# Kernel tuning notes

Hardware: AMD Instinct MI355X
Metric: run time of the kernel (lower is better)

The kernel has to match this reference:

```python
import jax, jax.numpy as jnp
import numpy as np

EPSILON = 1e-8
K = 3
PAD = K // 2


def setup_inputs() -> dict:
    key = jax.random.key(0)
    k1, k2, k3, k4 = jax.random.split(key, 4)
    B, FI, FO, H, W, DSTYLE = 8, 512, 512, 64, 64, 512
    return {
        "x": jax.random.normal(k1, (B, FI, H, W), dtype=jnp.float32),
        "style": jax.random.normal(k2, (B, DSTYLE), dtype=jnp.float32),
        "w": jax.random.normal(k3, (FO, FI, K, K), dtype=jnp.float32),
        "fc_w": jax.random.normal(k4, (FI, DSTYLE), dtype=jnp.float32),  # modLinear weight [dim_out=fi, dim_in=dim_style]
        "fc_b": jnp.zeros((FI,), dtype=jnp.float32),
    }


def reference(x, style, w, fc_w, fc_b):
    B, FI, H, W = x.shape
    FO = w.shape[0]
    DSTYLE = fc_w.shape[1]
    fc_scale = DSTYLE ** (-0.5)            # modLinear w_scale (lr_mult=1)
    w_scale = (FI * K * K) ** (-0.5)       # modConv w_scale

    # modLinear: style -> per-input-channel modulation s, shape [B, FI]
    s = style @ (fc_w * fc_scale).T + fc_b

    # Demod factor: d[b, fo] = rsqrt(sum_{fi,k,k} (w_scale * w * s[b,fi])^2 + eps)
    wsq = jnp.sum((w * w_scale) ** 2, axis=(2, 3))          # [FO, FI]
    d = jax.lax.rsqrt(jnp.einsum('of,bf->bo', wsq, s ** 2) + EPSILON)  # [B, FO]

    # Equivalent to per-sample grouped conv: scale input channels by s,
    # conv with shared base weight, scale output channels by demod.
    xm = x * s[:, :, None, None]
    y = jax.lax.conv_general_dilated(
        xm, w * w_scale,
        window_strides=(1, 1),
        padding=((PAD, PAD), (PAD, PAD)),
        dimension_numbers=('NCHW', 'OIHW', 'NCHW'),
    )
    return y * d[:, :, None, None]
```

## Files before the change

### kernel.cpp

```cpp
#include <hip/hip_runtime.h>


typedef __bf16 bf16_t;
typedef __bf16 bf16x8 __attribute__((ext_vector_type(8)));
typedef float floatx4 __attribute__((ext_vector_type(4)));

#define HW_ 4096
#define FCSCALE 0.04419417382415922f
#define WSCALE  0.014731391274719742f

#define VMCNT(n) asm volatile("s_waitcnt vmcnt(" #n ")" ::: "memory")

__device__ __forceinline__ void gload_lds16(const bf16_t* g, bf16_t* l) {
  __builtin_amdgcn_global_load_lds(
      (const __attribute__((address_space(1))) void*)g,
      (__attribute__((address_space(3))) void*)l, 16, 0, 0);
}


__device__ __forceinline__ void style_body(int bid, int t,
    const float* __restrict__ style, const float* __restrict__ fc_w,
    const float* __restrict__ fc_b, float* __restrict__ s_out) {
  int o = bid * 4 + (t >> 6);
  int lane = t & 63;
  int b = o >> 9, fi = o & 511;
  const float4* st = (const float4*)(style + b * 512);
  const float4* fw = (const float4*)(fc_w + (size_t)fi * 512);
  float4 a0 = st[lane * 2],     w0 = fw[lane * 2];
  float4 a1 = st[lane * 2 + 1], w1 = fw[lane * 2 + 1];
  float acc = a0.x * w0.x + a0.y * w0.y + a0.z * w0.z + a0.w * w0.w
            + a1.x * w1.x + a1.y * w1.y + a1.z * w1.z + a1.w * w1.w;
#pragma unroll
  for (int d = 32; d >= 1; d >>= 1) acc += __shfl_xor(acc, d, 64);
  if (lane == 0) s_out[o] = acc * FCSCALE + fc_b[fi];
}

__device__ __forceinline__ void wsq_wt_body(int bid, int t,
    const float* __restrict__ w, float* __restrict__ wsq, bf16_t* __restrict__ wt) {
  int idx = bid * 256 + t;
  int fo = idx >> 9, fi = idx & 511;
  const float* wp = w + (size_t)idx * 9;
  float v[9], q = 0.f;
#pragma unroll
  for (int k = 0; k < 9; ++k) { v[k] = wp[k] * WSCALE; q += v[k] * v[k]; }
  wsq[idx] = q;
#pragma unroll
  for (int k = 0; k < 9; ++k)
    wt[((((size_t)k * 64) + (fi >> 3)) * 512 + fo) * 8 + (fi & 7)] = (bf16_t)v[k];
}

__device__ __forceinline__ void demod_body(int bid, int t,
    const float* __restrict__ wsq, const float* __restrict__ s,
    float* __restrict__ dcoef) {
  int o = bid * 4 + (t >> 6);
  int lane = t & 63;
  int b = o >> 9, fo = o & 511;
  const float4* wq = (const float4*)(wsq + (size_t)fo * 512);
  const float4* sp = (const float4*)(s + b * 512);
  float acc = 0.f;
#pragma unroll
  for (int i = 0; i < 2; ++i) {
    float4 q = wq[lane * 2 + i], sv = sp[lane * 2 + i];
    acc += q.x * sv.x * sv.x + q.y * sv.y * sv.y + q.z * sv.z * sv.z + q.w * sv.w * sv.w;
  }
#pragma unroll
  for (int d = 32; d >= 1; d >>= 1) acc += __shfl_xor(acc, d, 64);
  if (lane == 0) dcoef[o] = rsqrtf(acc + 1e-8f);
}

__global__ void k_prep1(const float* __restrict__ style, const float* __restrict__ fc_w,
                        const float* __restrict__ fc_b, const float* __restrict__ w,
                        float* __restrict__ s_out, float* __restrict__ wsq,
                        bf16_t* __restrict__ wt, bf16_t* __restrict__ zerobuf) {
  int blk = blockIdx.x, t = threadIdx.x;
  if (blk < 1024) {
    wsq_wt_body(blk, t, w, wsq, wt);
  } else if (blk < 2048) {
    style_body(blk - 1024, t, style, fc_w, fc_b, s_out);
  } else {
    if (t < 128) zerobuf[t] = (bf16_t)0.f;
  }
}

__device__ __forceinline__ void modx_body(int fi0, int h, int b, int t,
    const float* __restrict__ x, const float* __restrict__ s,
    bf16_t* __restrict__ xT, float (*tile)[65]) {
  int c4 = (t & 15) * 4, fr = t >> 4;
#pragma unroll
  for (int i = 0; i < 2; ++i) {
    int fi_l = i * 16 + fr;
    float sv = s[b * 512 + fi0 + fi_l];
    float4 v = *(const float4*)(x + ((size_t)(b * 512 + fi0 + fi_l)) * HW_ + h * 64 + c4);
    tile[fi_l][c4] = v.x * sv; tile[fi_l][c4 + 1] = v.y * sv;
    tile[fi_l][c4 + 2] = v.z * sv; tile[fi_l][c4 + 3] = v.w * sv;
  }
  __syncthreads();
  int g_l = t >> 6, wcol = t & 63;
  bf16x8 vv;
#pragma unroll
  for (int j = 0; j < 8; ++j) vv[j] = (bf16_t)tile[g_l * 8 + j][wcol];
  *(bf16x8*)&xT[((((size_t)(b * 64 + h)) * 64 + (fi0 >> 3) + g_l) * 64 + wcol) * 8] = vv;
}

__global__ void k_prep2(const float* __restrict__ x, const float* __restrict__ s,
                        const float* __restrict__ wsq, float* __restrict__ dcoef,
                        bf16_t* __restrict__ xT) {
  __shared__ float tile[32][65];
  int blk = blockIdx.x, t = threadIdx.x;
  if (blk < 1024) {
    demod_body(blk, t, wsq, s, dcoef);
  } else {
    int m = blk - 1024;
    int b = m >> 10, rem = m & 1023;
    int h = rem >> 4, fi0 = (rem & 15) * 32;
    modx_body(fi0, h, b, t, x, s, xT, tile);
  }
}

__global__ __launch_bounds__(256, 2) void k_conv(const bf16_t* __restrict__ wt,
                                                 const bf16_t* __restrict__ xT,
                                                 const float* __restrict__ dcoef,
                                                 const bf16_t* __restrict__ zerobuf,
                                                 float* __restrict__ out) {
  __shared__ __align__(16) bf16_t sh[32776];

  int b   = blockIdx.x;
  int foB = blockIdx.y;
  int hq  = blockIdx.z;
  int t = threadIdx.x;
  int wv = t >> 6, lane = t & 63, quad = lane >> 4, l16 = lane & 15;
  int h0 = hq * 4;
  int fo_l = t & 127, chunk_hi = t >> 7;

  const bf16_t* xTb = xT + (size_t)b * 64 * 64 * 64 * 8;
  const bf16_t* zslotp = &sh[32768];
  int XRB = ((wv * 4 + quad) * 64 + l16) * 8;

  floatx4 acc[8][4];
#pragma unroll
  for (int i = 0; i < 8; ++i)
#pragma unroll
    for (int j = 0; j < 4; ++j) acc[i][j] = (floatx4){0.f, 0.f, 0.f, 0.f};

  if (t < 8) sh[32768 + t] = (bf16_t)0.f;
#pragma unroll
  for (int k = 0; k < 3; ++k)
#pragma unroll
    for (int u = 0; u < 2; ++u) {
      int s = k * 8 + wv * 2 + u;
      int r = s >> 2, g = s & 3;
      int rg = h0 + r - 1;
      const bf16_t* src = ((unsigned)rg < 64u)
          ? xTb + (((size_t)rg * 64 + g) * 64 + lane) * 8
          : zerobuf;
      gload_lds16(src, &sh[((r * 4 + g) * 64) * 8]);
    }
#pragma unroll
  for (int itw = 0; itw < 2; ++itw) {
    int cw = itw * 2 + chunk_hi;
    gload_lds16(wt + (((size_t)cw) * 512 + foB * 128 + fo_l) * 8,
                &sh[24576 + (itw * 256 + wv * 64) * 8]);
  }
  VMCNT(0);
  __syncthreads();

#define PHASE(P, NW, XPART, GCLAST)                                            \
  do {                                                                         \
    VMCNT(NW);                                                                 \
    __builtin_amdgcn_s_barrier();                                              \
    __builtin_amdgcn_sched_barrier(0);                                         \
    if (!(GCLAST) || (P) < 8) {        \
      const int TAP1 = ((P) + 1) % 9;                                          \
      int g01 = ((P) == 8) ? (gc + 1) * 4 : gc * 4;                            \
      int wb1 = ((gc9 + (P) + 1) & 1) * 4096;                                  \
      _Pragma("unroll")                                                        \
      for (int itw = 0; itw < 2; ++itw) {                                      \
        int cw = itw * 2 + chunk_hi;                                           \
        gload_lds16(wt + ((((size_t)TAP1 * 64) + g01 + cw) * 512               \
                          + foB * 128 + fo_l) * 8,                             \
                    &sh[24576 + wb1 + (itw * 256 + wv * 64) * 8]);             \
      }                                                                        \
    }                                                                          \
    if ((XPART) >= 0 && !(GCLAST)) { \
      int xb1 = ((gc + 1) & 1) * 12288;                                        \
      int g0n = (gc + 1) * 4;                                                  \
      _Pragma("unroll")                                                        \
      for (int u = 0; u < 2; ++u) {                                            \
        int s = (XPART) * 8 + wv * 2 + u;                                      \
        int r = s >> 2, g = s & 3;                                             \
        int rg = h0 + r - 1;                                                   \
        const bf16_t* src = ((unsigned)rg < 64u)                               \
            ? xTb + (((size_t)rg * 64 + g0n + g) * 64 + lane) * 8              \
            : zerobuf;                                                         \
        gload_lds16(src, &sh[xb1 + ((r * 4 + g) * 64) * 8]);                   \
      }                                                                        \
    }                                                                          \
    {                                  \
      const int KH = (P) / 3, KW = (P) % 3;                                    \
      int xb = (gc & 1) * 12288;                                               \
      int wb = ((gc9 + (P)) & 1) * 4096;                                       \
      bf16x8 bfr[4];                                                           \
      _Pragma("unroll")                                                        \
      for (int j = 0; j < 4; ++j) {                                            \
        const bf16_t* ap = &sh[xb + XRB + KH * 2048 + (j * 16 + KW - 1) * 8];  \
        if (KW == 0 && (j) == 0) { if (l16 == 0)  ap = zslotp; }               \
        if (KW == 2 && (j) == 3) { if (l16 == 15) ap = zslotp; }               \
        bfr[j] = *(const bf16x8*)ap;                                           \
      }                                                                        \
      __builtin_amdgcn_s_setprio(1);                                           \
      _Pragma("unroll")                                                        \
      for (int i = 0; i < 8; ++i) {                                            \
        bf16x8 afr = *(const bf16x8*)&sh[24576 + wb                            \
                                         + (quad * 128 + i * 16 + l16) * 8];   \
        _Pragma("unroll")                                                      \
        for (int j = 0; j < 4; ++j)                                            \
          acc[i][j] = __builtin_amdgcn_mfma_f32_16x16x32_bf16(                 \
              afr, bfr[j], acc[i][j], 0, 0, 0);                                \
      }                                                                        \
      __builtin_amdgcn_s_setprio(0);                                           \
    }                                                                          \
  } while (0)

  for (int gc = 0; gc < 15; ++gc) {
    int gc9 = gc * 9;
    PHASE(0, 0, -1, false);
    PHASE(1, 0,  0, false);
    PHASE(2, 2,  1, false);
    PHASE(3, 2,  2, false);
    PHASE(4, 2, -1, false);
    PHASE(5, 0, -1, false);
    PHASE(6, 0, -1, false);
    PHASE(7, 0, -1, false);
    PHASE(8, 0, -1, false);
  }
  {
    int gc = 15, gc9 = 135;
    PHASE(0, 0, -1, true);
    PHASE(1, 0, -1, true);
    PHASE(2, 0, -1, true);
    PHASE(3, 0, -1, true);
    PHASE(4, 0, -1, true);
    PHASE(5, 0, -1, true);
    PHASE(6, 0, -1, true);
    PHASE(7, 0, -1, true);
    PHASE(8, 0, -1, true);
  }
#undef PHASE

  int h = h0 + wv;
#pragma unroll
  for (int i = 0; i < 8; ++i) {
#pragma unroll
    for (int rr = 0; rr < 4; ++rr) {
      int fo_g = foB * 128 + i * 16 + quad * 4 + rr;
      float dm = dcoef[b * 512 + fo_g];
      float* op = out + ((size_t)((b * 512 + fo_g) * 64 + h)) * 64;
#pragma unroll
      for (int j = 0; j < 4; ++j)
        op[j * 16 + l16] = acc[i][j][rr] * dm;
    }
  }
}

extern "C" void kernel_launch(void* const* d_in, const int* in_sizes, int n_in,
                              void* d_out, int out_size, void* d_ws, size_t ws_size,
                              hipStream_t stream) {
  const float* x     = (const float*)d_in[0];
  const float* style = (const float*)d_in[1];
  const float* w     = (const float*)d_in[2];
  const float* fc_w  = (const float*)d_in[3];
  const float* fc_b  = (const float*)d_in[4];
  float* out = (float*)d_out;
  char* ws = (char*)d_ws;

  float*  s       = (float*)(ws);
  float*  dcoef   = (float*)(ws + 16384);
  float*  wsq     = (float*)(ws + 32768);
  bf16_t* zerobuf = (bf16_t*)(ws + 1081344);
  bf16_t* wt      = (bf16_t*)(ws + 1081600);
  bf16_t* xT      = (bf16_t*)(ws + 5800192);

  k_prep1<<<2049, 256, 0, stream>>>(style, fc_w, fc_b, w, s, wsq, wt, zerobuf);
  k_prep2<<<9216, 256, 0, stream>>>(x, s, wsq, dcoef, xT);
  k_conv<<<dim3(8, 4, 16), 256, 0, stream>>>(wt, xT, dcoef, zerobuf, out);
}
```

Baseline: 235.4 us.

## Stream conv weights into registers and retile waves to cut barriers

Weight fragments no longer go through LDS. Each wave loads them straight from global memory into a double-buffered register array, one tap ahead of the MFMA work. The waves are retiled as 2 output-channel halves by 2 row pairs, each wave holding 4x8 accumulators, and the workgroup barrier now runs only twice per pair of input-channel chunks instead of once per tap. This is meant to remove the per-tap barrier and LDS weight staging and to shrink LDS use. The cost is redundant global/L2 weight traffic across waves and exposed global-load latency in the register pipeline.

```diff
diff --git a/kernel.cpp b/kernel.cpp
--- a/kernel.cpp
+++ b/kernel.cpp
@@ -122,7 +122,7 @@
                                                  const float* __restrict__ dcoef,
                                                  const bf16_t* __restrict__ zerobuf,
                                                  float* __restrict__ out) {
-  __shared__ __align__(16) bf16_t sh[32776];
+  __shared__ __align__(16) bf16_t sh[24584];
 
   int b   = blockIdx.x;
   int foB = blockIdx.y;
@@ -130,25 +130,29 @@
   int t = threadIdx.x;
   int wv = t >> 6, lane = t & 63, quad = lane >> 4, l16 = lane & 15;
   int h0 = hq * 4;
-  int fo_l = t & 127, chunk_hi = t >> 7;
+  int rowpair = (wv >> 1) * 2;
+  int foW = foB * 128 + (wv & 1) * 64;
 
   const bf16_t* xTb = xT + (size_t)b * 64 * 64 * 64 * 8;
-  const bf16_t* zslotp = &sh[32768];
-  int XRB = ((wv * 4 + quad) * 64 + l16) * 8;
-
-  floatx4 acc[8][4];
-#pragma unroll
-  for (int i = 0; i < 8; ++i)
-#pragma unroll
-    for (int j = 0; j < 4; ++j) acc[i][j] = (floatx4){0.f, 0.f, 0.f, 0.f};
-
-  if (t < 8) sh[32768 + t] = (bf16_t)0.f;
-#pragma unroll
-  for (int k = 0; k < 3; ++k)
+  const bf16_t* wA_base = wt + ((size_t)(quad * 512 + foW + l16)) * 8;
+  const bf16_t* xlbase = &sh[(quad * 64 + l16) * 8];
+  const bf16_t* zslotp = &sh[24576];
+
+  floatx4 acc[4][8];
+#pragma unroll
+  for (int i = 0; i < 4; ++i)
+#pragma unroll
+    for (int j = 0; j < 8; ++j) acc[i][j] = (floatx4){0.f, 0.f, 0.f, 0.f};
+
+  bf16x8 aF[2][4];
+
+  if (t < 8) sh[24576 + t] = (bf16_t)0.f;
+#pragma unroll
+  for (int part = 0; part < 3; ++part)
 #pragma unroll
     for (int u = 0; u < 2; ++u) {
-      int s = k * 8 + wv * 2 + u;
-      int r = s >> 2, g = s & 3;
+      int sp = part * 8 + wv * 2 + u;
+      int r = sp >> 2, g = sp & 3;
       int rg = h0 + r - 1;
       const bf16_t* src = ((unsigned)rg < 64u)
           ? xTb + (((size_t)rg * 64 + g) * 64 + lane) * 8
@@ -156,108 +160,92 @@
       gload_lds16(src, &sh[((r * 4 + g) * 64) * 8]);
     }
 #pragma unroll
-  for (int itw = 0; itw < 2; ++itw) {
-    int cw = itw * 2 + chunk_hi;
-    gload_lds16(wt + (((size_t)cw) * 512 + foB * 128 + fo_l) * 8,
-                &sh[24576 + (itw * 256 + wv * 64) * 8]);
-  }
+  for (int i = 0; i < 4; ++i)
+    aF[0][i] = *(const bf16x8*)(wA_base + i * 128);
   VMCNT(0);
   __syncthreads();
 
-#define PHASE(P, NW, XPART, GCLAST)                                            \
+#define PH(IT18, LAST)                                                         \
   do {                                                                         \
-    VMCNT(NW);                                                                 \
-    __builtin_amdgcn_s_barrier();                                              \
-    __builtin_amdgcn_sched_barrier(0);                                         \
-    if (!(GCLAST) || (P) < 8) {        \
-      const int TAP1 = ((P) + 1) % 9;                                          \
-      int g01 = ((P) == 8) ? (gc + 1) * 4 : gc * 4;                            \
-      int wb1 = ((gc9 + (P) + 1) & 1) * 4096;                                  \
-      _Pragma("unroll")                                                        \
-      for (int itw = 0; itw < 2; ++itw) {                                      \
-        int cw = itw * 2 + chunk_hi;                                           \
-        gload_lds16(wt + ((((size_t)TAP1 * 64) + g01 + cw) * 512               \
-                          + foB * 128 + fo_l) * 8,                             \
-                    &sh[24576 + wb1 + (itw * 256 + wv * 64) * 8]);             \
-      }                                                                        \
-    }                                                                          \
-    if ((XPART) >= 0 && !(GCLAST)) { \
-      int xb1 = ((gc + 1) & 1) * 12288;                                        \
-      int g0n = (gc + 1) * 4;                                                  \
+    const int TAP_ = (IT18) % 9;                                               \
+    const int GH_  = (IT18) / 9;                                               \
+    if ((IT18) == 0 || (IT18) == 9) {                                          \
+      VMCNT(4);                                       \
+      __builtin_amdgcn_s_barrier();                 \
+      __builtin_amdgcn_sched_barrier(0);                                       \
+    }                                                                          \
+    if (TAP_ >= 3 && TAP_ <= 5 && !((LAST) && GH_ == 1)) {                     \
+      int gcn = gbase + GH_ + 1;                \
+      int xb1 = (gcn & 1) * 12288;                                             \
       _Pragma("unroll")                                                        \
       for (int u = 0; u < 2; ++u) {                                            \
-        int s = (XPART) * 8 + wv * 2 + u;                                      \
-        int r = s >> 2, g = s & 3;                                             \
+        int sp = (TAP_ - 3) * 8 + wv * 2 + u;                                  \
+        int r = sp >> 2, g = sp & 3;                                           \
         int rg = h0 + r - 1;                                                   \
         const bf16_t* src = ((unsigned)rg < 64u)                               \
-            ? xTb + (((size_t)rg * 64 + g0n + g) * 64 + lane) * 8              \
+            ? xTb + (((size_t)rg * 64 + gcn * 4 + g) * 64 + lane) * 8          \
             : zerobuf;                                                         \
         gload_lds16(src, &sh[xb1 + ((r * 4 + g) * 64) * 8]);                   \
       }                                                                        \
     }                                                                          \
-    {                                  \
-      const int KH = (P) / 3, KW = (P) % 3;                                    \
-      int xb = (gc & 1) * 12288;                                               \
-      int wb = ((gc9 + (P)) & 1) * 4096;                                       \
-      bf16x8 bfr[4];                                                           \
+    if (!((LAST) && (IT18) == 17)) {             \
+      const int T1 = ((IT18) + 1) % 9;                                         \
+      const int C1 = ((IT18) + 1) / 9;                                         \
+      const bf16_t* pA = wA_base + (size_t)(T1 * 64 + (gbase + C1) * 4) * 4096;\
       _Pragma("unroll")                                                        \
-      for (int j = 0; j < 4; ++j) {                                            \
-        const bf16_t* ap = &sh[xb + XRB + KH * 2048 + (j * 16 + KW - 1) * 8];  \
-        if (KW == 0 && (j) == 0) { if (l16 == 0)  ap = zslotp; }               \
-        if (KW == 2 && (j) == 3) { if (l16 == 15) ap = zslotp; }               \
-        bfr[j] = *(const bf16x8*)ap;                                           \
-      }                                                                        \
+      for (int i = 0; i < 4; ++i)                                              \
+        aF[((IT18) + 1) & 1][i] = *(const bf16x8*)(pA + i * 128);              \
+    }                                                                          \
+    {                                         \
+      const int KH_ = TAP_ / 3, KW_ = TAP_ % 3;                                \
+      const int XO_ = GH_ * 12288;                                             \
       __builtin_amdgcn_s_setprio(1);                                           \
       _Pragma("unroll")                                                        \
-      for (int i = 0; i < 8; ++i) {                                            \
-        bf16x8 afr = *(const bf16x8*)&sh[24576 + wb                            \
-                                         + (quad * 128 + i * 16 + l16) * 8];   \
+      for (int j = 0; j < 8; ++j) {                                            \
+        int r = rowpair + (j >> 2) + KH_;                                      \
+        const bf16_t* ap =                                                     \
+            xlbase + XO_ + r * 2048 + ((j & 3) * 16 + KW_ - 1) * 8;            \
+        if (KW_ == 0 && (j & 3) == 0) { if (l16 == 0)  ap = zslotp; }          \
+        if (KW_ == 2 && (j & 3) == 3) { if (l16 == 15) ap = zslotp; }          \
+        bf16x8 bfr = *(const bf16x8*)ap;                                       \
         _Pragma("unroll")                                                      \
-        for (int j = 0; j < 4; ++j)                                            \
+        for (int i = 0; i < 4; ++i)                                            \
           acc[i][j] = __builtin_amdgcn_mfma_f32_16x16x32_bf16(                 \
-              afr, bfr[j], acc[i][j], 0, 0, 0);                                \
+              aF[(IT18) & 1][i], bfr, acc[i][j], 0, 0, 0);                     \
       }                                                                        \
       __builtin_amdgcn_s_setprio(0);                                           \
     }                                                                          \
   } while (0)
 
-  for (int gc = 0; gc < 15; ++gc) {
-    int gc9 = gc * 9;
-    PHASE(0, 0, -1, false);
-    PHASE(1, 0,  0, false);
-    PHASE(2, 2,  1, false);
-    PHASE(3, 2,  2, false);
-    PHASE(4, 2, -1, false);
-    PHASE(5, 0, -1, false);
-    PHASE(6, 0, -1, false);
-    PHASE(7, 0, -1, false);
-    PHASE(8, 0, -1, false);
+  for (int gcp = 0; gcp < 7; ++gcp) {
+    int gbase = gcp * 2;
+    PH(0, false);  PH(1, false);  PH(2, false);  PH(3, false);  PH(4, false);
+    PH(5, false);  PH(6, false);  PH(7, false);  PH(8, false);  PH(9, false);
+    PH(10, false); PH(11, false); PH(12, false); PH(13, false); PH(14, false);
+    PH(15, false); PH(16, false); PH(17, false);
   }
   {
-    int gc = 15, gc9 = 135;
-    PHASE(0, 0, -1, true);
-    PHASE(1, 0, -1, true);
-    PHASE(2, 0, -1, true);
-    PHASE(3, 0, -1, true);
-    PHASE(4, 0, -1, true);
-    PHASE(5, 0, -1, true);
-    PHASE(6, 0, -1, true);
-    PHASE(7, 0, -1, true);
-    PHASE(8, 0, -1, true);
-  }
-#undef PHASE
-
-  int h = h0 + wv;
-#pragma unroll
-  for (int i = 0; i < 8; ++i) {
+    int gbase = 14;
+    PH(0, true);  PH(1, true);  PH(2, true);  PH(3, true);  PH(4, true);
+    PH(5, true);  PH(6, true);  PH(7, true);  PH(8, true);  PH(9, true);
+    PH(10, true); PH(11, true); PH(12, true); PH(13, true); PH(14, true);
+    PH(15, true); PH(16, true); PH(17, true);
+  }
+#undef PH
+
+#pragma unroll
+  for (int i = 0; i < 4; ++i) {
 #pragma unroll
     for (int rr = 0; rr < 4; ++rr) {
-      int fo_g = foB * 128 + i * 16 + quad * 4 + rr;
+      int fo_g = foW + i * 16 + quad * 4 + rr;
       float dm = dcoef[b * 512 + fo_g];
-      float* op = out + ((size_t)((b * 512 + fo_g) * 64 + h)) * 64;
-#pragma unroll
-      for (int j = 0; j < 4; ++j)
-        op[j * 16 + l16] = acc[i][j][rr] * dm;
+      float* op = out + ((size_t)(b * 512 + fo_g)) * 4096;
+#pragma unroll
+      for (int j = 0; j < 8; ++j) {
+        int h = h0 + rowpair + (j >> 2);
+        int c = (j & 3) * 16 + l16;
+        op[h * 64 + c] = acc[i][j][rr] * dm;
+      }
     }
   }
 }
```

Result: slower. 282.5 us (+20.0%).

## Double weight prefetch to two taps per barrier and unroll channel-group pairs

Applied to the files above, without the earlier changes.

Restructures the conv main loop so weight tiles for two taps are loaded together into a larger double-buffered LDS region, and a barrier is issued only every other MFMA phase. Two channel groups are processed per loop iteration, with x-tile prefetches rescheduled to match. The zero-slot pointer trick for boundary columns is replaced with wrapped LDS reads plus a register select of a zero vector. The aim is to halve barrier and wait overhead and deepen prefetch, at the cost of more LDS (80KB per block), which may lower occupancy from 2 blocks per CU.

```diff
diff --git a/kernel.cpp b/kernel.cpp
--- a/kernel.cpp
+++ b/kernel.cpp
@@ -122,7 +122,7 @@
                                                  const float* __restrict__ dcoef,
                                                  const bf16_t* __restrict__ zerobuf,
                                                  float* __restrict__ out) {
-  __shared__ __align__(16) bf16_t sh[32776];
+  __shared__ __align__(16) bf16_t sh[40960];
 
   int b   = blockIdx.x;
   int foB = blockIdx.y;
@@ -133,7 +133,6 @@
   int fo_l = t & 127, chunk_hi = t >> 7;
 
   const bf16_t* xTb = xT + (size_t)b * 64 * 64 * 64 * 8;
-  const bf16_t* zslotp = &sh[32768];
   int XRB = ((wv * 4 + quad) * 64 + l16) * 8;
 
   floatx4 acc[8][4];
@@ -142,13 +141,16 @@
 #pragma unroll
     for (int j = 0; j < 4; ++j) acc[i][j] = (floatx4){0.f, 0.f, 0.f, 0.f};
 
-  if (t < 8) sh[32768 + t] = (bf16_t)0.f;
-#pragma unroll
-  for (int k = 0; k < 3; ++k)
+  bf16x8 z8;
+#pragma unroll
+  for (int q = 0; q < 8; ++q) z8[q] = (bf16_t)0.f;
+
+#pragma unroll
+  for (int part = 0; part < 3; ++part)
 #pragma unroll
     for (int u = 0; u < 2; ++u) {
-      int s = k * 8 + wv * 2 + u;
-      int r = s >> 2, g = s & 3;
+      int sp = part * 8 + wv * 2 + u;
+      int r = sp >> 2, g = sp & 3;
       int rg = h0 + r - 1;
       const bf16_t* src = ((unsigned)rg < 64u)
           ? xTb + (((size_t)rg * 64 + g) * 64 + lane) * 8
@@ -156,62 +158,79 @@
       gload_lds16(src, &sh[((r * 4 + g) * 64) * 8]);
     }
 #pragma unroll
-  for (int itw = 0; itw < 2; ++itw) {
-    int cw = itw * 2 + chunk_hi;
-    gload_lds16(wt + (((size_t)cw) * 512 + foB * 128 + fo_l) * 8,
-                &sh[24576 + (itw * 256 + wv * 64) * 8]);
-  }
+  for (int half = 0; half < 2; ++half)
+#pragma unroll
+    for (int itw = 0; itw < 2; ++itw) {
+      int cw = itw * 2 + chunk_hi;
+      gload_lds16(wt + ((((size_t)half * 64) + cw) * 512 + foB * 128 + fo_l) * 8,
+                  &sh[24576 + half * 4096 + (itw * 256 + wv * 64) * 8]);
+    }
   VMCNT(0);
   __syncthreads();
 
-#define PHASE(P, NW, XPART, GCLAST)                                            \
+#define PH(P, NW, XPART, WST)                                                  \
   do {                                                                         \
-    VMCNT(NW);                                                                 \
-    __builtin_amdgcn_s_barrier();                                              \
-    __builtin_amdgcn_sched_barrier(0);                                         \
-    if (!(GCLAST) || (P) < 8) {        \
-      const int TAP1 = ((P) + 1) % 9;                                          \
-      int g01 = ((P) == 8) ? (gc + 1) * 4 : gc * 4;                            \
-      int wb1 = ((gc9 + (P) + 1) & 1) * 4096;                                  \
-      _Pragma("unroll")                                                        \
-      for (int itw = 0; itw < 2; ++itw) {                                      \
-        int cw = itw * 2 + chunk_hi;                                           \
-        gload_lds16(wt + ((((size_t)TAP1 * 64) + g01 + cw) * 512               \
-                          + foB * 128 + fo_l) * 8,                             \
-                    &sh[24576 + wb1 + (itw * 256 + wv * 64) * 8]);             \
-      }                                                                        \
-    }                                                                          \
-    if ((XPART) >= 0 && !(GCLAST)) { \
-      int xb1 = ((gc + 1) & 1) * 12288;                                        \
-      int g0n = (gc + 1) * 4;                                                  \
+    const int TAP_ = (P) % 9;                                                  \
+    const int GH_  = (P) / 9;                                                  \
+    if (((P) & 1) == 0) {                                                      \
+      VMCNT(NW);                                                               \
+      __builtin_amdgcn_s_barrier();                                            \
+      __builtin_amdgcn_sched_barrier(0);                                       \
+    }                                                                          \
+    if (WST) {                                  \
+      int wbo = 24576 + ((wsel ^ (((P) >> 1) & 1) ^ 1)) * 8192;                \
+      _Pragma("unroll")                                                        \
+      for (int half = 0; half < 2; ++half) {                                   \
+        const int PP = (P) + 2 + half;                                         \
+        const int T2 = PP % 9;                                                 \
+        const int GA = PP / 9;                                                 \
+        _Pragma("unroll")                                                      \
+        for (int itw = 0; itw < 2; ++itw) {                                    \
+          int cw = itw * 2 + chunk_hi;                                         \
+          gload_lds16(wt + ((((size_t)T2 * 64) + (gbase + GA) * 4 + cw) * 512  \
+                            + foB * 128 + fo_l) * 8,                           \
+                      &sh[wbo + half * 4096 + (itw * 256 + wv * 64) * 8]);     \
+        }                                                                      \
+      }                                                                        \
+    }                                                                          \
+    if ((XPART) >= 0) {                                \
+      int gcn = gbase + GH_ + 1;                                               \
+      int xb1 = (gcn & 1) * 12288;                                             \
       _Pragma("unroll")                                                        \
       for (int u = 0; u < 2; ++u) {                                            \
-        int s = (XPART) * 8 + wv * 2 + u;                                      \
-        int r = s >> 2, g = s & 3;                                             \
+        int sp = (XPART) * 8 + wv * 2 + u;                                     \
+        int r = sp >> 2, g = sp & 3;                                           \
         int rg = h0 + r - 1;                                                   \
         const bf16_t* src = ((unsigned)rg < 64u)                               \
-            ? xTb + (((size_t)rg * 64 + g0n + g) * 64 + lane) * 8              \
+            ? xTb + (((size_t)rg * 64 + gcn * 4 + g) * 64 + lane) * 8          \
             : zerobuf;                                                         \
         gload_lds16(src, &sh[xb1 + ((r * 4 + g) * 64) * 8]);                   \
       }                                                                        \
     }                                                                          \
-    {                                  \
-      const int KH = (P) / 3, KW = (P) % 3;                                    \
-      int xb = (gc & 1) * 12288;                                               \
-      int wb = ((gc9 + (P)) & 1) * 4096;                                       \
+    {                                            \
+      const int KH_ = TAP_ / 3, KW_ = TAP_ % 3;                                \
+      const int XO_ = GH_ * 12288;                                             \
+      int wb = 24576 + (wsel ^ (((P) >> 1) & 1)) * 8192 + ((P) & 1) * 4096;    \
       bf16x8 bfr[4];                                                           \
       _Pragma("unroll")                                                        \
       for (int j = 0; j < 4; ++j) {                                            \
-        const bf16_t* ap = &sh[xb + XRB + KH * 2048 + (j * 16 + KW - 1) * 8];  \
-        if (KW == 0 && (j) == 0) { if (l16 == 0)  ap = zslotp; }               \
-        if (KW == 2 && (j) == 3) { if (l16 == 15) ap = zslotp; }               \
-        bfr[j] = *(const bf16x8*)ap;                                           \
+        if (KW_ == 0 && j == 0) {                                              \
+          bfr[0] = *(const bf16x8*)&sh[XO_ +                                   \
+              (((wv + KH_) * 4 + quad) * 64 + ((l16 + 63) & 63)) * 8];         \
+          bfr[0] = (l16 == 0) ? z8 : bfr[0];                                   \
+        } else if (KW_ == 2 && j == 3) {                                       \
+          bfr[3] = *(const bf16x8*)&sh[XO_ +                                   \
+              (((wv + KH_) * 4 + quad) * 64 + ((l16 + 49) & 63)) * 8];         \
+          bfr[3] = (l16 == 15) ? z8 : bfr[3];                                  \
+        } else {                                                               \
+          bfr[j] = *(const bf16x8*)&sh[XRB + XO_ + KH_ * 2048 +                \
+                                       (j * 16 + KW_ - 1) * 8];                \
+        }                                                                      \
       }                                                                        \
       __builtin_amdgcn_s_setprio(1);                                           \
       _Pragma("unroll")                                                        \
       for (int i = 0; i < 8; ++i) {                                            \
-        bf16x8 afr = *(const bf16x8*)&sh[24576 + wb                            \
-                                         + (quad * 128 + i * 16 + l16) * 8];   \
+        bf16x8 afr = *(const bf16x8*)&sh[wb + (quad * 128 + i * 16 + l16) * 8];\
         _Pragma("unroll")                                                      \
         for (int j = 0; j < 4; ++j)                                            \
           acc[i][j] = __builtin_amdgcn_mfma_f32_16x16x32_bf16(                 \
@@ -221,31 +240,25 @@
     }                                                                          \
   } while (0)
 
-  for (int gc = 0; gc < 15; ++gc) {
-    int gc9 = gc * 9;
-    PHASE(0, 0, -1, false);
-    PHASE(1, 0,  0, false);
-    PHASE(2, 2,  1, false);
-    PHASE(3, 2,  2, false);
-    PHASE(4, 2, -1, false);
-    PHASE(5, 0, -1, false);
-    PHASE(6, 0, -1, false);
-    PHASE(7, 0, -1, false);
-    PHASE(8, 0, -1, false);
+  for (int gcp = 0; gcp < 7; ++gcp) {
+    int gbase = gcp * 2;
+    int wsel = gcp & 1;
+    PH(0, 0, -1, 1);  PH(1, 0, -1, 0);  PH(2, 0, -1, 1);  PH(3, 0, 0, 0);
+    PH(4, 2, 1, 1);   PH(5, 0, 2, 0);   PH(6, 4, -1, 1);  PH(7, 0, -1, 0);
+    PH(8, 0, -1, 1);  PH(9, 0, -1, 0);  PH(10, 0, -1, 1); PH(11, 0, -1, 0);
+    PH(12, 0, 0, 1);  PH(13, 0, 1, 0);  PH(14, 4, 2, 1);  PH(15, 0, -1, 0);
+    PH(16, 2, -1, 1); PH(17, 0, -1, 0);
   }
   {
-    int gc = 15, gc9 = 135;
-    PHASE(0, 0, -1, true);
-    PHASE(1, 0, -1, true);
-    PHASE(2, 0, -1, true);
-    PHASE(3, 0, -1, true);
-    PHASE(4, 0, -1, true);
-    PHASE(5, 0, -1, true);
-    PHASE(6, 0, -1, true);
-    PHASE(7, 0, -1, true);
-    PHASE(8, 0, -1, true);
-  }
-#undef PHASE
+    int gbase = 14;
+    int wsel = 1;
+    PH(0, 0, -1, 1);  PH(1, 0, -1, 0);  PH(2, 0, -1, 1);  PH(3, 0, 0, 0);
+    PH(4, 2, 1, 1);   PH(5, 0, 2, 0);   PH(6, 4, -1, 1);  PH(7, 0, -1, 0);
+    PH(8, 0, -1, 1);  PH(9, 0, -1, 0);  PH(10, 0, -1, 1); PH(11, 0, -1, 0);
+    PH(12, 0, -1, 1); PH(13, 0, -1, 0); PH(14, 0, -1, 1); PH(15, 0, -1, 0);
+    PH(16, 0, -1, 0); PH(17, 0, -1, 0);
+  }
+#undef PH
 
   int h = h0 + wv;
 #pragma unroll
```

Result: no change. 235.6 us (+0.1%).

## Merge prep kernels and compute demod coefficients inside the conv kernel

Applied to the files above, without the earlier changes.

The two preprocessing launches become one: x-modulation blocks now recompute their own slice of the style modulation s locally instead of waiting on a separate kernel, and each block handles four rows. The demodulation factors are no longer precomputed; each conv block computes its 128 factors from wsq and s in its prologue, staged through LDS. This drops one kernel launch and the dependency between launches, at the cost of redundant style dot products per block and extra prologue work and LDS in the conv kernel.

```diff
diff --git a/kernel.cpp b/kernel.cpp
--- a/kernel.cpp
+++ b/kernel.cpp
@@ -49,80 +49,74 @@
     wt[((((size_t)k * 64) + (fi >> 3)) * 512 + fo) * 8 + (fi & 7)] = (bf16_t)v[k];
 }
 
-__device__ __forceinline__ void demod_body(int bid, int t,
-    const float* __restrict__ wsq, const float* __restrict__ s,
-    float* __restrict__ dcoef) {
-  int o = bid * 4 + (t >> 6);
-  int lane = t & 63;
-  int b = o >> 9, fo = o & 511;
-  const float4* wq = (const float4*)(wsq + (size_t)fo * 512);
-  const float4* sp = (const float4*)(s + b * 512);
-  float acc = 0.f;
+__device__ __forceinline__ void modx_body_loc(int fi0, int h, int b, int t,
+    const float* __restrict__ x, const float* __restrict__ s_loc,
+    bf16_t* __restrict__ xT, float (*tile)[65]) {
+  int c4 = (t & 15) * 4, fr = t >> 4;
 #pragma unroll
   for (int i = 0; i < 2; ++i) {
-    float4 q = wq[lane * 2 + i], sv = sp[lane * 2 + i];
-    acc += q.x * sv.x * sv.x + q.y * sv.y * sv.y + q.z * sv.z * sv.z + q.w * sv.w * sv.w;
-  }
-#pragma unroll
-  for (int d = 32; d >= 1; d >>= 1) acc += __shfl_xor(acc, d, 64);
-  if (lane == 0) dcoef[o] = rsqrtf(acc + 1e-8f);
-}
-
-__global__ void k_prep1(const float* __restrict__ style, const float* __restrict__ fc_w,
-                        const float* __restrict__ fc_b, const float* __restrict__ w,
-                        float* __restrict__ s_out, float* __restrict__ wsq,
-                        bf16_t* __restrict__ wt, bf16_t* __restrict__ zerobuf) {
+    int fi_l = i * 16 + fr;
+    float sv = s_loc[fi_l];
+    float4 v = *(const float4*)(x + ((size_t)(b * 512 + fi0 + fi_l)) * HW_ + h * 64 + c4);
+    tile[fi_l][c4] = v.x * sv; tile[fi_l][c4 + 1] = v.y * sv;
+    tile[fi_l][c4 + 2] = v.z * sv; tile[fi_l][c4 + 3] = v.w * sv;
+  }
+  __syncthreads();
+  int g_l = t >> 6, wcol = t & 63;
+  bf16x8 vv;
+#pragma unroll
+  for (int j = 0; j < 8; ++j) vv[j] = (bf16_t)tile[g_l * 8 + j][wcol];
+  *(bf16x8*)&xT[((((size_t)(b * 64 + h)) * 64 + (fi0 >> 3) + g_l) * 64 + wcol) * 8] = vv;
+}
+
+__global__ void k_prep(const float* __restrict__ style, const float* __restrict__ fc_w,
+                       const float* __restrict__ fc_b, const float* __restrict__ w,
+                       const float* __restrict__ x,
+                       float* __restrict__ s_out, float* __restrict__ wsq,
+                       bf16_t* __restrict__ wt, bf16_t* __restrict__ zerobuf,
+                       bf16_t* __restrict__ xT) {
+  __shared__ float tile[32][65];
+  __shared__ float s_loc[32];
   int blk = blockIdx.x, t = threadIdx.x;
   if (blk < 1024) {
     wsq_wt_body(blk, t, w, wsq, wt);
   } else if (blk < 2048) {
     style_body(blk - 1024, t, style, fc_w, fc_b, s_out);
+  } else if (blk == 2048) {
+    if (t < 128) zerobuf[t] = (bf16_t)0.f;
   } else {
-    if (t < 128) zerobuf[t] = (bf16_t)0.f;
-  }
-}
-
-__device__ __forceinline__ void modx_body(int fi0, int h, int b, int t,
-    const float* __restrict__ x, const float* __restrict__ s,
-    bf16_t* __restrict__ xT, float (*tile)[65]) {
-  int c4 = (t & 15) * 4, fr = t >> 4;
-#pragma unroll
-  for (int i = 0; i < 2; ++i) {
-    int fi_l = i * 16 + fr;
-    float sv = s[b * 512 + fi0 + fi_l];
-    float4 v = *(const float4*)(x + ((size_t)(b * 512 + fi0 + fi_l)) * HW_ + h * 64 + c4);
-    tile[fi_l][c4] = v.x * sv; tile[fi_l][c4 + 1] = v.y * sv;
-    tile[fi_l][c4 + 2] = v.z * sv; tile[fi_l][c4 + 3] = v.w * sv;
-  }
-  __syncthreads();
-  int g_l = t >> 6, wcol = t & 63;
-  bf16x8 vv;
-#pragma unroll
-  for (int j = 0; j < 8; ++j) vv[j] = (bf16_t)tile[g_l * 8 + j][wcol];
-  *(bf16x8*)&xT[((((size_t)(b * 64 + h)) * 64 + (fi0 >> 3) + g_l) * 64 + wcol) * 8] = vv;
-}
-
-__global__ void k_prep2(const float* __restrict__ x, const float* __restrict__ s,
-                        const float* __restrict__ wsq, float* __restrict__ dcoef,
-                        bf16_t* __restrict__ xT) {
-  __shared__ float tile[32][65];
-  int blk = blockIdx.x, t = threadIdx.x;
-  if (blk < 1024) {
-    demod_body(blk, t, wsq, s, dcoef);
-  } else {
-    int m = blk - 1024;
-    int b = m >> 10, rem = m & 1023;
-    int h = rem >> 4, fi0 = (rem & 15) * 32;
-    modx_body(fi0, h, b, t, x, s, xT, tile);
+    int m = blk - 2049;
+    int b = m >> 8, rem = m & 255;
+    int hq = rem >> 4, fi0 = (rem & 15) * 32;
+    int fi_l = t >> 3, part = t & 7;
+    const float4* st4 = (const float4*)(style + b * 512);
+    const float4* fw4 = (const float4*)(fc_w + (size_t)(fi0 + fi_l) * 512);
+    float a = 0.f;
+#pragma unroll
+    for (int i = 0; i < 16; ++i) {
+      float4 sv = st4[part * 16 + i], wv = fw4[part * 16 + i];
+      a += sv.x * wv.x + sv.y * wv.y + sv.z * wv.z + sv.w * wv.w;
+    }
+    a += __shfl_xor(a, 1, 64);
+    a += __shfl_xor(a, 2, 64);
+    a += __shfl_xor(a, 4, 64);
+    if (part == 0) s_loc[fi_l] = a * FCSCALE + fc_b[fi0 + fi_l];
+    __syncthreads();
+#pragma unroll
+    for (int h4 = 0; h4 < 4; ++h4) {
+      modx_body_loc(fi0, hq * 4 + h4, b, t, x, s_loc, xT, tile);
+      __syncthreads();
+    }
   }
 }
 
 __global__ __launch_bounds__(256, 2) void k_conv(const bf16_t* __restrict__ wt,
                                                  const bf16_t* __restrict__ xT,
-                                                 const float* __restrict__ dcoef,
+                                                 const float* __restrict__ s,
+                                                 const float* __restrict__ wsq,
                                                  const bf16_t* __restrict__ zerobuf,
                                                  float* __restrict__ out) {
-  __shared__ __align__(16) bf16_t sh[32776];
+  __shared__ __align__(16) bf16_t sh[34056];
 
   int b   = blockIdx.x;
   int foB = blockIdx.y;
@@ -134,6 +128,8 @@
 
   const bf16_t* xTb = xT + (size_t)b * 64 * 64 * 64 * 8;
   const bf16_t* zslotp = &sh[32768];
+  float* s_lds = (float*)&sh[32776];
+  float* d_lds = (float*)&sh[33800];
   int XRB = ((wv * 4 + quad) * 64 + l16) * 8;
 
   floatx4 acc[8][4];
@@ -147,8 +143,8 @@
   for (int k = 0; k < 3; ++k)
 #pragma unroll
     for (int u = 0; u < 2; ++u) {
-      int s = k * 8 + wv * 2 + u;
-      int r = s >> 2, g = s & 3;
+      int sp = k * 8 + wv * 2 + u;
+      int r = sp >> 2, g = sp & 3;
       int rg = h0 + r - 1;
       const bf16_t* src = ((unsigned)rg < 64u)
           ? xTb + (((size_t)rg * 64 + g) * 64 + lane) * 8
@@ -160,6 +156,25 @@
     int cw = itw * 2 + chunk_hi;
     gload_lds16(wt + (((size_t)cw) * 512 + foB * 128 + fo_l) * 8,
                 &sh[24576 + (itw * 256 + wv * 64) * 8]);
+  }
+  if (t < 128)
+    ((float4*)s_lds)[t] = ((const float4*)(s + b * 512))[t];
+  asm volatile("s_waitcnt lgkmcnt(0)" ::: "memory");
+  __builtin_amdgcn_s_barrier();
+  __builtin_amdgcn_sched_barrier(0);
+  {
+    int fo_h = t >> 1, half = t & 1;
+    const float4* wq = (const float4*)(wsq + (size_t)(foB * 128 + fo_h) * 512) + half * 64;
+    const float4* sp4 = ((const float4*)s_lds) + half * 64;
+    float a = 0.f;
+#pragma unroll 8
+    for (int i = 0; i < 64; ++i) {
+      float4 q = wq[i], sv = sp4[i];
+      a += q.x * sv.x * sv.x + q.y * sv.y * sv.y
+         + q.z * sv.z * sv.z + q.w * sv.w * sv.w;
+    }
+    a += __shfl_xor(a, 1, 64);
+    if (half == 0) d_lds[fo_h] = rsqrtf(a + 1e-8f);
   }
   VMCNT(0);
   __syncthreads();
@@ -186,8 +201,8 @@
       int g0n = (gc + 1) * 4;                                                  \
       _Pragma("unroll")                                                        \
       for (int u = 0; u < 2; ++u) {                                            \
-        int s = (XPART) * 8 + wv * 2 + u;                                      \
-        int r = s >> 2, g = s & 3;                                             \
+        int sp = (XPART) * 8 + wv * 2 + u;                                     \
+        int r = sp >> 2, g = sp & 3;                                           \
         int rg = h0 + r - 1;                                                   \
         const bf16_t* src = ((unsigned)rg < 64u)                               \
             ? xTb + (((size_t)rg * 64 + g0n + g) * 64 + lane) * 8              \
@@ -252,9 +267,9 @@
   for (int i = 0; i < 8; ++i) {
 #pragma unroll
     for (int rr = 0; rr < 4; ++rr) {
-      int fo_g = foB * 128 + i * 16 + quad * 4 + rr;
-      float dm = dcoef[b * 512 + fo_g];
-      float* op = out + ((size_t)((b * 512 + fo_g) * 64 + h)) * 64;
+      int fo_loc = i * 16 + quad * 4 + rr;
+      float dm = d_lds[fo_loc];
+      float* op = out + ((size_t)((b * 512 + foB * 128 + fo_loc) * 64 + h)) * 64;
 #pragma unroll
       for (int j = 0; j < 4; ++j)
         op[j * 16 + l16] = acc[i][j][rr] * dm;
@@ -274,13 +289,11 @@
   char* ws = (char*)d_ws;
 
   float*  s       = (float*)(ws);
-  float*  dcoef   = (float*)(ws + 16384);
   float*  wsq     = (float*)(ws + 32768);
   bf16_t* zerobuf = (bf16_t*)(ws + 1081344);
   bf16_t* wt      = (bf16_t*)(ws + 1081600);
   bf16_t* xT      = (bf16_t*)(ws + 5800192);
 
-  k_prep1<<<2049, 256, 0, stream>>>(style, fc_w, fc_b, w, s, wsq, wt, zerobuf);
-  k_prep2<<<9216, 256, 0, stream>>>(x, s, wsq, dcoef, xT);
-  k_conv<<<dim3(8, 4, 16), 256, 0, stream>>>(wt, xT, dcoef, zerobuf, out);
-}
+  k_prep<<<4097, 256, 0, stream>>>(style, fc_w, fc_b, w, x, s, wsq, wt, zerobuf, xT);
+  k_conv<<<dim3(8, 4, 16), 256, 0, stream>>>(wt, xT, s, wsq, zerobuf, out);
+}
```

After: 273.4 us. 16.1% more time.
